# Kernel optimization log

Hardware: AMD Instinct MI355X
Metric: run time of the kernel (lower is better)

Reference implementation:

```python
import math
import jax, jax.numpy as jnp
import numpy as np

N_HEAD = 16
ROPE_BASE = 10000.0

def setup_inputs() -> dict:
    key = jax.random.key(0)
    k1, k2, k3 = jax.random.split(key, 3)
    B, T, C = 2, 2048, 2048
    x = jax.random.normal(k1, (B, T, C), dtype=jnp.float32)
    Wqkv = jax.random.normal(k2, (C, 3 * C), dtype=jnp.float32) * 0.02  # [C, 3C], y = x @ Wqkv
    Wout = jax.random.normal(k3, (C, C), dtype=jnp.float32) * 0.02
    return {"x": x, "Wqkv": Wqkv, "Wout": Wout}

def _rope_sin_cos(T, half, dtype):
    # build_sin_cos(seq_len, dim=head_size//2): div over arange(0, 2*dim, 2) / (2*dim)
    pos = jnp.arange(T, dtype=jnp.float32)[:, None]                      # [T,1]
    div = jnp.exp(jnp.arange(0, 2 * half, 2, dtype=jnp.float32)
                  * (-math.log(ROPE_BASE) / (2 * half)))                 # [half]
    ang = pos * div                                                      # [T,half]
    return jnp.sin(ang).astype(dtype), jnp.cos(ang).astype(dtype)

def reference(x, Wqkv, Wout):
    B, T, C = x.shape
    H = N_HEAD
    D = C // H
    half = D // 2
    qkv = (x @ Wqkv).reshape(B, T, 3, H, D)
    q, k, v = qkv[:, :, 0], qkv[:, :, 1], qkv[:, :, 2]                   # [B,T,H,D]
    sin, cos = _rope_sin_cos(T, half, x.dtype)
    sin = sin[None, :, None, :]  # [1,T,1,half]
    cos = cos[None, :, None, :]
    def rope(t):
        t1, t2 = t[..., :half], t[..., half:]
        return jnp.concatenate([t1 * cos - t2 * sin, t2 * cos + t1 * sin], axis=-1)
    q, k = rope(q), rope(k)
    scale = 1.0 / math.sqrt(D)  # flash-attn default softmax_scale
    scores = jnp.einsum('bthd,bshd->bhts', q, k) * scale                 # [B,H,T,T]
    causal = jnp.tril(jnp.ones((T, T), dtype=bool))
    scores = jnp.where(causal[None, None], scores, jnp.finfo(scores.dtype).min)
    probs = jax.nn.softmax(scores, axis=-1)
    out = jnp.einsum('bhts,bshd->bhtd', probs, v)                        # [B,H,T,D]
    # Faithful to torch: out.permute(0,2,1,3).reshape(B,T,C) on [B,T,H,D]
    # == flatten of [B,H,T,D] into [B,T,C]
    out = out.reshape(B, T, C)
    return out @ Wout
```

## Files before the change

### kernel.cpp

```cpp
#include <hip/hip_runtime.h>

typedef unsigned short u16;
typedef __attribute__((ext_vector_type(8))) short bf16x8;
typedef __attribute__((ext_vector_type(4))) float f32x4;
typedef __attribute__((ext_vector_type(8))) unsigned short u16x8;

#define B_ 2
#define T_ 2048
#define C_ 2048
#define H_ 16
#define D_ 128
#define QKVW 6144

__device__ __forceinline__ u16 f2b(float f) {
  unsigned int x = __builtin_bit_cast(unsigned int, f);
  x += 0x7fffu + ((x >> 16) & 1u);
  return (u16)(x >> 16);
}
__device__ __forceinline__ float b2f(u16 u) {
  unsigned int x = ((unsigned int)u) << 16;
  return __builtin_bit_cast(float, x);
}
__device__ __forceinline__ void gl_lds16(const void* g, void* l) {
  __builtin_amdgcn_global_load_lds((const __attribute__((address_space(1))) void*)g,
                                   (__attribute__((address_space(3))) void*)l, 16, 0, 0);
}

__global__ void castbf(const float* __restrict__ in, u16* __restrict__ out) {
  int i = blockIdx.x * 256 + threadIdx.x;
  f32x4 a = ((const f32x4*)in)[2 * i];
  f32x4 b = ((const f32x4*)in)[2 * i + 1];
  u16x8 o;
  o[0] = f2b(a[0]); o[1] = f2b(a[1]); o[2] = f2b(a[2]); o[3] = f2b(a[3]);
  o[4] = f2b(b[0]); o[5] = f2b(b[1]); o[6] = f2b(b[2]); o[7] = f2b(b[3]);
  ((u16x8*)out)[i] = o;
}

__global__ __launch_bounds__(256) void castT(const float* __restrict__ in,
                                             u16* __restrict__ out, int K, int N) {
  __shared__ __align__(16) u16 ld[64][72];
  const int nt = blockIdx.x * 64, kt = blockIdx.y * 64;
  const int tid = threadIdx.x;
#pragma unroll
  for (int s = 0; s < 4; ++s) {
    int idx = tid + s * 256;
    int r = idx >> 4;
    int c = (idx & 15) * 4;
    f32x4 v = *(const f32x4*)(in + (size_t)(kt + r) * N + nt + c);
    ld[r][c] = f2b(v[0]); ld[r][c + 1] = f2b(v[1]);
    ld[r][c + 2] = f2b(v[2]); ld[r][c + 3] = f2b(v[3]);
  }
  __syncthreads();
#pragma unroll
  for (int s = 0; s < 2; ++s) {
    int idx = tid + s * 256;
    int n = idx >> 3;
    int c8 = (idx & 7) * 8;
    u16x8 o;
#pragma unroll
    for (int j = 0; j < 8; ++j) o[j] = ld[c8 + j][n];
    *(u16x8*)(out + (size_t)(nt + n) * K + kt + c8) = o;
  }
}

__device__ __forceinline__ void stage_chunk(const u16* __restrict__ g, int K,
                                            u16* l, int ch) {
  int row = ch >> 3;
  int c = (ch & 7) ^ (row & 7);
  gl_lds16(g + (size_t)row * K + c * 8, l + ch * 8);
}

#define MFMA_Q(AF, BF, MH, NH)                                               \
  _Pragma("unroll")                                                          \
  for (int mi = 0; mi < 4; ++mi) {                                           \
    _Pragma("unroll")                                                        \
    for (int ni = 0; ni < 2; ++ni) {                                         \
      _Pragma("unroll")                                                      \
      for (int ks = 0; ks < 2; ++ks)                                         \
        acc[(MH)*4 + mi][(NH)*2 + ni] =                                      \
            __builtin_amdgcn_mfma_f32_16x16x32_bf16(                         \
                AF[mi][ks], BF[ni][ks], acc[(MH)*4 + mi][(NH)*2 + ni],       \
                0, 0, 0);                                                    \
    }                                                                        \
  }

template <int OUT_BF16>
__global__ __launch_bounds__(512, 2) void gemm256(const u16* __restrict__ A,
                                                  const u16* __restrict__ Bt,
                                                  void* __restrict__ Cout,
                                                  int M, int N, int K) {
  __shared__ __align__(16) u16 sm[65536];
  const int tid = threadIdx.x;
  const int lane = tid & 63, w = tid >> 6;
  const int quad = lane >> 4, l15 = lane & 15;
  const int wm = w >> 2, wn = w & 3;
  const int NXT = N >> 8;
  int id = blockIdx.x;
  const int cpx = gridDim.x >> 3;
  id = (id & 7) * cpx + (id >> 3);
  const int tn0 = (id % NXT) * 256, tm0 = (id / NXT) * 256;
  const int NT = K >> 6;
  const u16* Ag = A + (size_t)tm0 * K;
  const u16* Bg = Bt + (size_t)tn0 * K;

  f32x4 acc[8][4] = {};
  bf16x8 a0[4][2], a1[4][2], b0[2][2], b1[2][2];

  auto stA = [&](int tt, int half) {
    u16* l = &sm[(tt & 1) * 32768];
    const u16* g = Ag + tt * 64;
    stage_chunk(g, K, l, half * 512 + tid);
    stage_chunk(g, K, l, 1024 + half * 512 + tid);
  };
  auto stB = [&](int tt, int nh) {
    u16* l = &sm[(tt & 1) * 32768 + 16384];
    const u16* g = Bg + tt * 64;
    int ch = nh * 256 + (tid & 255) + ((tid >> 8) << 9);
    stage_chunk(g, K, l, ch);
    stage_chunk(g, K, l, ch + 1024);
  };

  stA(0, 0); stB(0, 0); stA(0, 1); stB(0, 1);
  if (NT > 1) {
    stA(1, 0); stB(1, 0); stA(1, 1);
    asm volatile("s_waitcnt vmcnt(6)" ::: "memory");
  } else {
    asm volatile("s_waitcnt vmcnt(0)" ::: "memory");
  }
  __builtin_amdgcn_s_barrier();

  for (int t = 0; t < NT; ++t) {
    const u16* LA = &sm[(t & 1) * 32768];
    const u16* LB = LA + 16384;
#pragma unroll
    for (int mi = 0; mi < 4; ++mi)
#pragma unroll
      for (int ks = 0; ks < 2; ++ks) {
        int r = wm * 128 + mi * 16 + l15;
        a0[mi][ks] = *(const bf16x8*)&LA[r * 64 +
                     ((ks * 32 + quad * 8) ^ ((r & 7) << 3))];
      }
#pragma unroll
    for (int ni = 0; ni < 2; ++ni)
#pragma unroll
      for (int ks = 0; ks < 2; ++ks) {
        int r = wn * 64 + ni * 16 + l15;
        b0[ni][ks] = *(const bf16x8*)&LB[r * 64 +
                     ((ks * 32 + quad * 8) ^ ((r & 7) << 3))];
      }
    if (t + 1 < NT) stB(t + 1, 1);
    __builtin_amdgcn_s_barrier();
    asm volatile("s_waitcnt lgkmcnt(0)");
    __builtin_amdgcn_sched_barrier(0);
    __builtin_amdgcn_s_setprio(1);
    MFMA_Q(a0, b0, 0, 0);
    __builtin_amdgcn_s_setprio(0);
    __builtin_amdgcn_s_barrier();
#pragma unroll
    for (int ni = 0; ni < 2; ++ni)
#pragma unroll
      for (int ks = 0; ks < 2; ++ks) {
        int r = wn * 64 + (ni + 2) * 16 + l15;
        b1[ni][ks] = *(const bf16x8*)&LB[r * 64 +
                     ((ks * 32 + quad * 8) ^ ((r & 7) << 3))];
      }
    if (t + 2 < NT) stA(t + 2, 0);
    __builtin_amdgcn_s_barrier();
    asm volatile("s_waitcnt lgkmcnt(0)");
    __builtin_amdgcn_sched_barrier(0);
    __builtin_amdgcn_s_setprio(1);
    MFMA_Q(a0, b1, 0, 1);
    __builtin_amdgcn_s_setprio(0);
    __builtin_amdgcn_s_barrier();
#pragma unroll
    for (int mi = 0; mi < 4; ++mi)
#pragma unroll
      for (int ks = 0; ks < 2; ++ks) {
        int r = wm * 128 + (mi + 4) * 16 + l15;
        a1[mi][ks] = *(const bf16x8*)&LA[r * 64 +
                     ((ks * 32 + quad * 8) ^ ((r & 7) << 3))];
      }
    if (t + 2 < NT) stB(t + 2, 0);
    __builtin_amdgcn_s_barrier();
    asm volatile("s_waitcnt lgkmcnt(0)");
    __builtin_amdgcn_sched_barrier(0);
    __builtin_amdgcn_s_setprio(1);
    MFMA_Q(a1, b1, 1, 1);
    __builtin_amdgcn_s_setprio(0);
    __builtin_amdgcn_s_barrier();
    if (t + 2 < NT) {
      stA(t + 2, 1);
      asm volatile("s_waitcnt vmcnt(6)" ::: "memory");
    } else {
      asm volatile("s_waitcnt vmcnt(0)" ::: "memory");
    }
    __builtin_amdgcn_s_barrier();
    __builtin_amdgcn_s_setprio(1);
    MFMA_Q(a1, b0, 1, 0);
    __builtin_amdgcn_s_setprio(0);
    __builtin_amdgcn_s_barrier();
  }

#pragma unroll
  for (int mi = 0; mi < 8; ++mi)
#pragma unroll
    for (int ni = 0; ni < 4; ++ni)
#pragma unroll
      for (int r = 0; r < 4; ++r) {
        int row = tm0 + wm * 128 + mi * 16 + quad * 4 + r;
        int col = tn0 + wn * 64 + ni * 16 + l15;
        float v = acc[mi][ni][r];
        if (OUT_BF16) ((u16*)Cout)[(size_t)row * N + col] = f2b(v);
        else          ((float*)Cout)[(size_t)row * N + col] = v;
      }
}

__global__ void rope_k(u16* __restrict__ qkv) {
  int idx = blockIdx.x * 256 + threadIdx.x;
  int i = idx & 63;
  int h = (idx >> 6) & 15;
  int which = (idx >> 10) & 1;
  int t = (idx >> 11) & 2047;
  int b = idx >> 22;
  size_t base = (size_t)(b * T_ + t) * QKVW + which * 2048 + h * 128 + i;
  float t1 = b2f(qkv[base]), t2 = b2f(qkv[base + 64]);
  float ang = (float)t * exp2f(-(float)i * 0.20762050593046439f);
  float sn, cs;
  sincosf(ang, &sn, &cs);
  qkv[base]      = f2b(t1 * cs - t2 * sn);
  qkv[base + 64] = f2b(t2 * cs + t1 * sn);
}

__global__ __launch_bounds__(256) void vtrans(const u16* __restrict__ qkv, u16* __restrict__ vt) {
  __shared__ __align__(16) u16 ld[128][136];
  const int tt = blockIdx.x, bh = blockIdx.y;
  const int b = bh >> 4, h = bh & 15;
  const u16* vb = qkv + (size_t)b * T_ * QKVW + 4096 + h * 128;
  const int tid = threadIdx.x;
#pragma unroll
  for (int s = 0; s < 8; ++s) {
    int t = (tid >> 4) + s * 16;
    int d0 = (tid & 15) * 8;
    *(bf16x8*)&ld[t][d0] = *(const bf16x8*)(vb + (size_t)(tt * 128 + t) * QKVW + d0);
  }
  __syncthreads();
  u16* vout = vt + (size_t)bh * D_ * T_ + tt * 128;
#pragma unroll
  for (int s = 0; s < 8; ++s) {
    int d = (tid >> 4) + s * 16;
    int t0 = (tid & 15) * 8;
    u16x8 o;
#pragma unroll
    for (int j = 0; j < 8; ++j) o[j] = ld[t0 + j][d];
    *(u16x8*)(vout + (size_t)d * T_ + t0) = o;
  }
}

#define APW 72
__global__ __launch_bounds__(256, 2) void attn(const u16* __restrict__ qkv,
                                               const u16* __restrict__ vt,
                                               u16* __restrict__ obuf) {
  __shared__ __align__(16) u16 lK[2][64 * 128];
  __shared__ __align__(16) u16 lV[2][128 * 64];
  __shared__ __align__(16) u16 lP[64 * APW];
  const int tid = threadIdx.x, lane = tid & 63, w = tid >> 6;
  const int quad = lane >> 4, l15 = lane & 15;
  const int bh = blockIdx.x, jp = blockIdx.y;
  const int jA = jp, jB = 31 - jp;
  const int b = bh >> 4, h = bh & 15;
  const u16* qb = qkv + (size_t)b * T_ * QKVW + h * 128;
  const u16* kb = qb + 2048;
  const u16* vtb = vt + (size_t)bh * D_ * T_;

  bf16x8 qfA[4], qfB[4];
#pragma unroll
  for (int kk = 0; kk < 4; ++kk) {
    qfA[kk] = *(const bf16x8*)(qb + (size_t)(jA * 64 + w * 16 + l15) * QKVW + kk * 32 + quad * 8);
    qfB[kk] = *(const bf16x8*)(qb + (size_t)(jB * 64 + w * 16 + l15) * QKVW + kk * 32 + quad * 8);
  }

  f32x4 oA[8] = {}, oB[8] = {};
  float mA[4], lAr[4], mB[4], lBr[4];
#pragma unroll
  for (int r = 0; r < 4; ++r) {
    mA[r] = -__builtin_inff(); lAr[r] = 0.f;
    mB[r] = -__builtin_inff(); lBr[r] = 0.f;
  }
  const float sc = 0.08838834764831845f * 1.4426950408889634f;

  auto stage = [&](int kt, int buf) {
#pragma unroll
    for (int s = 0; s < 4; ++s) {
      int ch = tid + s * 256;
      int kr = ch >> 4, kc = (ch & 15) ^ (kr & 7);
      gl_lds16(kb + (size_t)(kt * 64 + kr) * QKVW + kc * 8, &lK[buf][ch * 8]);
      int vr = ch >> 3, vc = (ch & 7) ^ (vr & 7);
      gl_lds16(vtb + (size_t)vr * T_ + kt * 64 + vc * 8, &lV[buf][ch * 8]);
    }
  };

  auto tile_compute = [&](const bf16x8* qf, f32x4* oacc, float* mrow, float* lrow,
                          int jw, int kt, int cb) {
    f32x4 sacc[4] = {};
#pragma unroll
    for (int kk = 0; kk < 4; ++kk) {
      bf16x8 kf[4];
#pragma unroll
      for (int nj = 0; nj < 4; ++nj) {
        int r = nj * 16 + l15;
        kf[nj] = *(const bf16x8*)&lK[cb][r * 128 + ((kk * 32 + quad * 8) ^ ((r & 7) << 3))];
      }
      __builtin_amdgcn_s_setprio(1);
#pragma unroll
      for (int nj = 0; nj < 4; ++nj)
        sacc[nj] = __builtin_amdgcn_mfma_f32_16x16x32_bf16(qf[kk], kf[nj], sacc[nj], 0, 0, 0);
      __builtin_amdgcn_s_setprio(0);
    }
    const bool diag = (kt == jw);
#pragma unroll
    for (int nj = 0; nj < 4; ++nj) {
      int key = nj * 16 + l15;
#pragma unroll
      for (int r = 0; r < 4; ++r) {
        float s = sacc[nj][r] * sc;
        if (diag) {
          int qrow = w * 16 + quad * 4 + r;
          if (key > qrow) s = -__builtin_inff();
        }
        sacc[nj][r] = s;
      }
    }
    float pm[4];
#pragma unroll
    for (int r = 0; r < 4; ++r)
      pm[r] = fmaxf(fmaxf(sacc[0][r], sacc[1][r]), fmaxf(sacc[2][r], sacc[3][r]));
    float dmax = fmaxf(fmaxf(pm[0] - mrow[0], pm[1] - mrow[1]),
                       fmaxf(pm[2] - mrow[2], pm[3] - mrow[3]));
    if (__any(dmax > 11.5f)) {
#pragma unroll
      for (int r = 0; r < 4; ++r) {
        float rm = pm[r];
        rm = fmaxf(rm, __shfl_xor(rm, 1));
        rm = fmaxf(rm, __shfl_xor(rm, 2));
        rm = fmaxf(rm, __shfl_xor(rm, 4));
        rm = fmaxf(rm, __shfl_xor(rm, 8));
        float mold = mrow[r];
        float mnew = fmaxf(mold, rm);
        float alpha = exp2f(mold - mnew);
#pragma unroll
        for (int nd = 0; nd < 8; ++nd) oacc[nd][r] *= alpha;
        lrow[r] *= alpha;
        mrow[r] = mnew;
      }
    }
#pragma unroll
    for (int r = 0; r < 4; ++r) {
      int prow = w * 16 + quad * 4 + r;
      float rs = 0.f;
#pragma unroll
      for (int nj = 0; nj < 4; ++nj) {
        float p = exp2f(sacc[nj][r] - mrow[r]);
        rs += p;
        lP[prow * APW + nj * 16 + l15] = f2b(p);
      }
      lrow[r] += rs;
    }
#pragma unroll
    for (int kk = 0; kk < 2; ++kk) {
      bf16x8 pf, vf[8];
      pf = *(const bf16x8*)&lP[(w * 16 + l15) * APW + kk * 32 + quad * 8];
#pragma unroll
      for (int nd = 0; nd < 8; ++nd) {
        int r = nd * 16 + l15;
        vf[nd] = *(const bf16x8*)&lV[cb][r * 64 + ((kk * 32 + quad * 8) ^ ((r & 7) << 3))];
      }
      __builtin_amdgcn_s_setprio(1);
#pragma unroll
      for (int nd = 0; nd < 8; ++nd)
        oacc[nd] = __builtin_amdgcn_mfma_f32_16x16x32_bf16(pf, vf[nd], oacc[nd], 0, 0, 0);
      __builtin_amdgcn_s_setprio(0);
    }
  };

  stage(0, 0);
  __syncthreads();

  for (int kt = 0; kt <= jB; ++kt) {
    int cb = kt & 1;
    if (kt < jB) stage(kt + 1, cb ^ 1);
    tile_compute(qfB, oB, mB, lBr, jB, kt, cb);
    if (kt <= jA) tile_compute(qfA, oA, mA, lAr, jA, kt, cb);
    __syncthreads();
  }

#pragma unroll
  for (int r = 0; r < 4; ++r) {
    float sA = lAr[r], sB = lBr[r];
    sA += __shfl_xor(sA, 1); sB += __shfl_xor(sB, 1);
    sA += __shfl_xor(sA, 2); sB += __shfl_xor(sB, 2);
    sA += __shfl_xor(sA, 4); sB += __shfl_xor(sB, 4);
    sA += __shfl_xor(sA, 8); sB += __shfl_xor(sB, 8);
    lAr[r] = sA; lBr[r] = sB;
  }

#pragma unroll
  for (int nd = 0; nd < 8; ++nd)
#pragma unroll
    for (int r = 0; r < 4; ++r) {
      int dcol = nd * 16 + l15;
      int qrB = jB * 64 + w * 16 + quad * 4 + r;
      obuf[((size_t)bh * T_ + qrB) * D_ + dcol] = f2b(oB[nd][r] / lBr[r]);
      int qrA = jA * 64 + w * 16 + quad * 4 + r;
      obuf[((size_t)bh * T_ + qrA) * D_ + dcol] = f2b(oA[nd][r] / lAr[r]);
    }
}

extern "C" void kernel_launch(void* const* d_in, const int* in_sizes, int n_in,
                              void* d_out, int out_size, void* d_ws, size_t ws_size,
                              hipStream_t stream) {
  const float* x = (const float*)d_in[0];
  const float* Wqkv = (const float*)d_in[1];
  const float* Wout = (const float*)d_in[2];
  float* out = (float*)d_out;
  char* ws = (char*)d_ws;

  u16* xb   = (u16*)ws;
  u16* wqt  = (u16*)(ws + 16777216);
  u16* qkvb = (u16*)(ws + 41943040);
  u16* vtb  = (u16*)(ws + 92274688);
  u16* wot  = wqt;
  u16* ob   = xb;

  castbf<<<4096, 256, 0, stream>>>(x, xb);
  castT<<<dim3(96, 32), 256, 0, stream>>>(Wqkv, wqt, 2048, 6144);
  gemm256<1><<<dim3(384), 512, 0, stream>>>(xb, wqt, qkvb, 4096, 6144, 2048);
  castT<<<dim3(32, 32), 256, 0, stream>>>(Wout, wot, 2048, 2048);
  rope_k<<<32768, 256, 0, stream>>>(qkvb);
  vtrans<<<dim3(16, 32), 256, 0, stream>>>(qkvb, vtb);
  attn<<<dim3(32, 16), 256, 0, stream>>>(qkvb, vtb, ob);
  gemm256<0><<<dim3(128), 512, 0, stream>>>(ob, wot, out, 4096, 2048, 2048);
}
```

Before: 410.6 us.

## Replace 256x256 GEMM with 128x256 tile, K=32 steps and new LDS layout

Rewrites the GEMM kernel to use 128x256 output tiles with a 32-wide K step and a quad-major LDS layout in place of the XOR-swizzled 64-wide layout, and doubles the grid sizes. Smaller tiles and a smaller LDS footprint (48KB) allow four blocks per CU and more blocks for the 2048-wide output projection, which had only 128 blocks on a 256-CU device. The cost is lower arithmetic intensity per tile, twice as many barrier-separated K iterations, and possible LDS bank conflicts from the unswizzled layout.

```diff
diff --git a/kernel.cpp b/kernel.cpp
--- a/kernel.cpp
+++ b/kernel.cpp
@@ -63,33 +63,12 @@
   }
 }
 
-__device__ __forceinline__ void stage_chunk(const u16* __restrict__ g, int K,
-                                            u16* l, int ch) {
-  int row = ch >> 3;
-  int c = (ch & 7) ^ (row & 7);
-  gl_lds16(g + (size_t)row * K + c * 8, l + ch * 8);
-}
-
-#define MFMA_Q(AF, BF, MH, NH)                                               \
-  _Pragma("unroll")                                                          \
-  for (int mi = 0; mi < 4; ++mi) {                                           \
-    _Pragma("unroll")                                                        \
-    for (int ni = 0; ni < 2; ++ni) {                                         \
-      _Pragma("unroll")                                                      \
-      for (int ks = 0; ks < 2; ++ks)                                         \
-        acc[(MH)*4 + mi][(NH)*2 + ni] =                                      \
-            __builtin_amdgcn_mfma_f32_16x16x32_bf16(                         \
-                AF[mi][ks], BF[ni][ks], acc[(MH)*4 + mi][(NH)*2 + ni],       \
-                0, 0, 0);                                                    \
-    }                                                                        \
-  }
-
 template <int OUT_BF16>
-__global__ __launch_bounds__(512, 2) void gemm256(const u16* __restrict__ A,
+__global__ __launch_bounds__(512, 4) void gemm128(const u16* __restrict__ A,
                                                   const u16* __restrict__ Bt,
                                                   void* __restrict__ Cout,
                                                   int M, int N, int K) {
-  __shared__ __align__(16) u16 sm[65536];
+  __shared__ __align__(16) u16 sm[2][12288];
   const int tid = threadIdx.x;
   const int lane = tid & 63, w = tid >> 6;
   const int quad = lane >> 4, l15 = lane & 15;
@@ -98,118 +77,108 @@
   int id = blockIdx.x;
   const int cpx = gridDim.x >> 3;
   id = (id & 7) * cpx + (id >> 3);
-  const int tn0 = (id % NXT) * 256, tm0 = (id / NXT) * 256;
-  const int NT = K >> 6;
+  const int tn0 = (id % NXT) * 256, tm0 = (id / NXT) * 128;
+  const int NT = K >> 5;
   const u16* Ag = A + (size_t)tm0 * K;
   const u16* Bg = Bt + (size_t)tn0 * K;
 
-  f32x4 acc[8][4] = {};
-  bf16x8 a0[4][2], a1[4][2], b0[2][2], b1[2][2];
-
-  auto stA = [&](int tt, int half) {
-    u16* l = &sm[(tt & 1) * 32768];
-    const u16* g = Ag + tt * 64;
-    stage_chunk(g, K, l, half * 512 + tid);
-    stage_chunk(g, K, l, 1024 + half * 512 + tid);
+  f32x4 acc[4][4] = {};
+  bf16x8 a0[2], a1[2], b0[2], b1[2];
+
+  const int aq = tid >> 7, aidx = tid & 127;
+  const int ahalf = aidx >> 6, apr = aidx & 63;
+  const int arow = (apr >> 5) * 64 + ahalf * 32 + (apr & 31);
+  const int bq = tid >> 7, bpr = tid & 127;
+  const int brow0 = (bpr >> 5) * 64 + (bpr & 31);
+
+  auto stA = [&](int t) {
+    gl_lds16(Ag + (size_t)arow * K + t * 32 + aq * 8, &sm[t & 1][tid * 8]);
   };
-  auto stB = [&](int tt, int nh) {
-    u16* l = &sm[(tt & 1) * 32768 + 16384];
-    const u16* g = Bg + tt * 64;
-    int ch = nh * 256 + (tid & 255) + ((tid >> 8) << 9);
-    stage_chunk(g, K, l, ch);
-    stage_chunk(g, K, l, ch + 1024);
+  auto stB = [&](int t, int half) {
+    gl_lds16(Bg + (size_t)(brow0 + half * 32) * K + t * 32 + bq * 8,
+             &sm[t & 1][4096 + bq * 2048 + half * 1024 + bpr * 8]);
   };
 
-  stA(0, 0); stB(0, 0); stA(0, 1); stB(0, 1);
-  if (NT > 1) {
-    stA(1, 0); stB(1, 0); stA(1, 1);
-    asm volatile("s_waitcnt vmcnt(6)" ::: "memory");
-  } else {
-    asm volatile("s_waitcnt vmcnt(0)" ::: "memory");
-  }
+  stA(0); stB(0, 0); stB(0, 1);
+  asm volatile("s_waitcnt vmcnt(1)" ::: "memory");
   __builtin_amdgcn_s_barrier();
 
   for (int t = 0; t < NT; ++t) {
-    const u16* LA = &sm[(t & 1) * 32768];
-    const u16* LB = LA + 16384;
-#pragma unroll
-    for (int mi = 0; mi < 4; ++mi)
-#pragma unroll
-      for (int ks = 0; ks < 2; ++ks) {
-        int r = wm * 128 + mi * 16 + l15;
-        a0[mi][ks] = *(const bf16x8*)&LA[r * 64 +
-                     ((ks * 32 + quad * 8) ^ ((r & 7) << 3))];
-      }
-#pragma unroll
-    for (int ni = 0; ni < 2; ++ni)
-#pragma unroll
-      for (int ks = 0; ks < 2; ++ks) {
-        int r = wn * 64 + ni * 16 + l15;
-        b0[ni][ks] = *(const bf16x8*)&LB[r * 64 +
-                     ((ks * 32 + quad * 8) ^ ((r & 7) << 3))];
-      }
-    if (t + 1 < NT) stB(t + 1, 1);
+    const u16* L = &sm[t & 1][0];
+#pragma unroll
+    for (int mi = 0; mi < 2; ++mi)
+      a0[mi] = *(const bf16x8*)&L[quad * 1024 + (wm * 32 + mi * 16 + l15) * 8];
+#pragma unroll
+    for (int nj = 0; nj < 2; ++nj)
+      b0[nj] = *(const bf16x8*)&L[4096 + quad * 2048 + (wn * 32 + nj * 16 + l15) * 8];
+    if (t + 1 < NT) {
+      stA(t + 1);
+      asm volatile("s_waitcnt vmcnt(1)" ::: "memory");
+    } else {
+      asm volatile("s_waitcnt vmcnt(0)" ::: "memory");
+    }
     __builtin_amdgcn_s_barrier();
     asm volatile("s_waitcnt lgkmcnt(0)");
     __builtin_amdgcn_sched_barrier(0);
     __builtin_amdgcn_s_setprio(1);
-    MFMA_Q(a0, b0, 0, 0);
+#pragma unroll
+    for (int mi = 0; mi < 2; ++mi)
+#pragma unroll
+      for (int nj = 0; nj < 2; ++nj)
+        acc[mi][nj] = __builtin_amdgcn_mfma_f32_16x16x32_bf16(a0[mi], b0[nj], acc[mi][nj], 0, 0, 0);
     __builtin_amdgcn_s_setprio(0);
     __builtin_amdgcn_s_barrier();
 #pragma unroll
-    for (int ni = 0; ni < 2; ++ni)
-#pragma unroll
-      for (int ks = 0; ks < 2; ++ks) {
-        int r = wn * 64 + (ni + 2) * 16 + l15;
-        b1[ni][ks] = *(const bf16x8*)&LB[r * 64 +
-                     ((ks * 32 + quad * 8) ^ ((r & 7) << 3))];
-      }
-    if (t + 2 < NT) stA(t + 2, 0);
+    for (int nj = 0; nj < 2; ++nj)
+      b1[nj] = *(const bf16x8*)&L[4096 + quad * 2048 + 1024 + (wn * 32 + nj * 16 + l15) * 8];
+    if (t + 1 < NT) stB(t + 1, 0);
     __builtin_amdgcn_s_barrier();
     asm volatile("s_waitcnt lgkmcnt(0)");
     __builtin_amdgcn_sched_barrier(0);
     __builtin_amdgcn_s_setprio(1);
-    MFMA_Q(a0, b1, 0, 1);
+#pragma unroll
+    for (int mi = 0; mi < 2; ++mi)
+#pragma unroll
+      for (int nj = 0; nj < 2; ++nj)
+        acc[mi][nj + 2] = __builtin_amdgcn_mfma_f32_16x16x32_bf16(a0[mi], b1[nj], acc[mi][nj + 2], 0, 0, 0);
     __builtin_amdgcn_s_setprio(0);
     __builtin_amdgcn_s_barrier();
 #pragma unroll
-    for (int mi = 0; mi < 4; ++mi)
-#pragma unroll
-      for (int ks = 0; ks < 2; ++ks) {
-        int r = wm * 128 + (mi + 4) * 16 + l15;
-        a1[mi][ks] = *(const bf16x8*)&LA[r * 64 +
-                     ((ks * 32 + quad * 8) ^ ((r & 7) << 3))];
-      }
-    if (t + 2 < NT) stB(t + 2, 0);
+    for (int mi = 0; mi < 2; ++mi)
+      a1[mi] = *(const bf16x8*)&L[quad * 1024 + 512 + (wm * 32 + mi * 16 + l15) * 8];
+    if (t + 1 < NT) stB(t + 1, 1);
     __builtin_amdgcn_s_barrier();
     asm volatile("s_waitcnt lgkmcnt(0)");
     __builtin_amdgcn_sched_barrier(0);
     __builtin_amdgcn_s_setprio(1);
-    MFMA_Q(a1, b1, 1, 1);
+#pragma unroll
+    for (int mi = 0; mi < 2; ++mi)
+#pragma unroll
+      for (int nj = 0; nj < 2; ++nj)
+        acc[mi + 2][nj + 2] = __builtin_amdgcn_mfma_f32_16x16x32_bf16(a1[mi], b1[nj], acc[mi + 2][nj + 2], 0, 0, 0);
     __builtin_amdgcn_s_setprio(0);
     __builtin_amdgcn_s_barrier();
-    if (t + 2 < NT) {
-      stA(t + 2, 1);
-      asm volatile("s_waitcnt vmcnt(6)" ::: "memory");
-    } else {
-      asm volatile("s_waitcnt vmcnt(0)" ::: "memory");
-    }
-    __builtin_amdgcn_s_barrier();
     __builtin_amdgcn_s_setprio(1);
-    MFMA_Q(a1, b0, 1, 0);
+#pragma unroll
+    for (int mi = 0; mi < 2; ++mi)
+#pragma unroll
+      for (int nj = 0; nj < 2; ++nj)
+        acc[mi + 2][nj] = __builtin_amdgcn_mfma_f32_16x16x32_bf16(a1[mi], b0[nj], acc[mi + 2][nj], 0, 0, 0);
     __builtin_amdgcn_s_setprio(0);
-    __builtin_amdgcn_s_barrier();
-  }
-
-#pragma unroll
-  for (int mi = 0; mi < 8; ++mi)
-#pragma unroll
-    for (int ni = 0; ni < 4; ++ni)
+    if (t + 1 < NT)
+      asm volatile("s_waitcnt vmcnt(1)" ::: "memory");
+    __builtin_amdgcn_s_barrier();
+  }
+
+#pragma unroll
+  for (int mi = 0; mi < 4; ++mi)
+#pragma unroll
+    for (int nj = 0; nj < 4; ++nj)
 #pragma unroll
       for (int r = 0; r < 4; ++r) {
-        int row = tm0 + wm * 128 + mi * 16 + quad * 4 + r;
-        int col = tn0 + wn * 64 + ni * 16 + l15;
-        float v = acc[mi][ni][r];
+        int row = tm0 + wm * 64 + mi * 16 + quad * 4 + r;
+        int col = tn0 + wn * 64 + nj * 16 + l15;
+        float v = acc[mi][nj][r];
         if (OUT_BF16) ((u16*)Cout)[(size_t)row * N + col] = f2b(v);
         else          ((float*)Cout)[(size_t)row * N + col] = v;
       }
@@ -433,10 +402,10 @@
 
   castbf<<<4096, 256, 0, stream>>>(x, xb);
   castT<<<dim3(96, 32), 256, 0, stream>>>(Wqkv, wqt, 2048, 6144);
-  gemm256<1><<<dim3(384), 512, 0, stream>>>(xb, wqt, qkvb, 4096, 6144, 2048);
+  gemm128<1><<<dim3(768), 512, 0, stream>>>(xb, wqt, qkvb, 4096, 6144, 2048);
   castT<<<dim3(32, 32), 256, 0, stream>>>(Wout, wot, 2048, 2048);
   rope_k<<<32768, 256, 0, stream>>>(qkvb);
   vtrans<<<dim3(16, 32), 256, 0, stream>>>(qkvb, vtb);
   attn<<<dim3(32, 16), 256, 0, stream>>>(qkvb, vtb, ob);
-  gemm256<0><<<dim3(128), 512, 0, stream>>>(ob, wot, out, 4096, 2048, 2048);
-}
+  gemm128<0><<<dim3(256), 512, 0, stream>>>(ob, wot, out, 4096, 2048, 2048);
+}
```

New measurement: 455.5 us. +10.9%, slower.
